# Kernel optimization log

Measured on AMD Instinct MI355X. Metric: run time of the kernel, lower is better.

The kernel has to match this reference:

```python
import jax, jax.numpy as jnp
import numpy as np


def _proj(W, b, x):
    # 1x1 conv == per-pixel GEMM over channels: [O,C] x [B,C,H,W] -> [B,O,H,W]
    return jnp.einsum('oc,bchw->bohw', W, x) + b[None, :, None, None]


def _cross(src, ctx, Wq, bq, Wk, bk, Wv, bv):
    # queries from src, keys/values from ctx; returns [B,C,H,W]
    B, C, H, W = src.shape
    HW = H * W
    q = _proj(Wq, bq, src).reshape(B, -1, HW)   # [B, C//8, HW]
    k = _proj(Wk, bk, ctx).reshape(B, -1, HW)   # [B, C//8, HW]
    v = _proj(Wv, bv, ctx).reshape(B, C, HW)    # [B, C,    HW]
    # attn[b,i,j] = softmax_j( q[b,:,i] . k[b,:,j] )
    attn = jax.nn.softmax(jnp.einsum('bci,bcj->bij', q, k), axis=-1)
    out = jnp.einsum('bcj,bij->bci', v, attn)   # [B, C, HW]
    return out.reshape(B, C, H, W)


def setup_inputs() -> dict:
    key = jax.random.key(0)
    ks = jax.random.split(key, 8)
    dim = 256
    B, H, W = 4, 64, 64
    return {
        'x': jax.random.normal(ks[0], (B, dim, H, W), jnp.float32),
        'y': jax.random.normal(ks[1], (B, dim, H, W), jnp.float32),
        'Wq': jax.random.normal(ks[2], (dim // 8, dim), jnp.float32) * 0.05,
        'bq': jax.random.normal(ks[3], (dim // 8,), jnp.float32) * 0.05,
        'Wk': jax.random.normal(ks[4], (dim // 8, dim), jnp.float32) * 0.05,
        'bk': jax.random.normal(ks[5], (dim // 8,), jnp.float32) * 0.05,
        'Wv': jax.random.normal(ks[6], (dim, dim), jnp.float32) * 0.05,
        'bv': jax.random.normal(ks[7], (dim,), jnp.float32) * 0.05,
    }


def reference(x, y, Wq, bq, Wk, bk, Wv, bv):
    outx = _cross(x, y, Wq, bq, Wk, bk, Wv, bv)  # x queries attend to y
    outy = _cross(y, x, Wq, bq, Wk, bk, Wv, bv)  # y queries attend to x
    return (outx, outy)
```

## Files before the change

### kernel.cpp

```cpp
#include <hip/hip_runtime.h>

#define BB 4
#define CC 256
#define DD 32
#define SS 4096

typedef __bf16 bf16;
typedef __bf16 bf16x8 __attribute__((ext_vector_type(8)));
typedef __bf16 bf16x4 __attribute__((ext_vector_type(4)));
typedef float f32x4 __attribute__((ext_vector_type(4)));
typedef unsigned int u32;
typedef u32 u32x4 __attribute__((ext_vector_type(4)));
typedef unsigned short u16;

#define Q_OFF  0
#define K_OFF  1048576
#define V_OFF  2097152
#define WB_OFF 10485760
#define CH_ELEM 16384

static __device__ __forceinline__ u32 pack2(float lo, float hi) {
    bf16 a = (bf16)lo, b = (bf16)hi;
    u16 ua = __builtin_bit_cast(u16, a), ub = __builtin_bit_cast(u16, b);
    return (u32)ua | ((u32)ub << 16);
}

static __device__ __forceinline__ void bar_vm12() {
    asm volatile("s_waitcnt vmcnt(12)" ::: "memory");
    __builtin_amdgcn_s_barrier();
    asm volatile("" ::: "memory");
}
static __device__ __forceinline__ void bar_plain() {
    asm volatile("" ::: "memory");
    __builtin_amdgcn_s_barrier();
    asm volatile("" ::: "memory");
}

__global__ __launch_bounds__(256) void prep_kernel(
    const float* __restrict__ x, const float* __restrict__ y,
    const float* __restrict__ Wq, const float* __restrict__ Wk,
    const float* __restrict__ Wv,
    bf16* __restrict__ xb, bf16* __restrict__ wb)
{
    const int t   = threadIdx.x;
    const int bid = blockIdx.x;

    if (bid >= 512) {
        const int gid = (bid - 512)*256 + t;
        const int idx = gid*8;
        const int o = idx >> 8, cc = idx & 255;
        const float* row = (o < 32) ? (Wq + (size_t)o*CC)
                         : (o < 64) ? (Wk + (size_t)(o-32)*CC)
                                    : (Wv + (size_t)(o-64)*CC);
        const float4 a = *(const float4*)(row + cc);
        const float4 c = *(const float4*)(row + cc + 4);
        bf16x8 pk;
        pk[0]=(bf16)a.x; pk[1]=(bf16)a.y; pk[2]=(bf16)a.z; pk[3]=(bf16)a.w;
        pk[4]=(bf16)c.x; pk[5]=(bf16)c.y; pk[6]=(bf16)c.z; pk[7]=(bf16)c.w;
        *(bf16x8*)(wb + idx) = pk;
        return;
    }

    const int dirb = bid & 7;
    const int src  = dirb >> 2;
    const int b    = dirb & 3;
    const int tile = bid >> 3;
    const float* in = (src ? y : x) + (size_t)b*CC*SS + tile*64;
    bf16* outp = xb + (size_t)dirb*1048576 + (size_t)tile*CH_ELEM;

    const int ln    = t & 15;
    const int quadf = (t >> 4) & 3;
    const int w     = t >> 6;
    #pragma unroll
    for (int cop = 0; cop < 2; ++cop) {
        const int co = w*2 + cop;
        #pragma unroll
        for (int pb = 0; pb < 4; ++pb) {
            float f[8];
            #pragma unroll
            for (int j = 0; j < 8; ++j)
                f[j] = in[(size_t)(8*quadf + 32*co + j)*SS + pb*16 + ln];
            bf16x8 pk;
            #pragma unroll
            for (int j = 0; j < 8; ++j) pk[j] = (bf16)f[j];
            *(bf16x8*)(outp + pb*4096 + co*512 + quadf*128 + ln*8) = pk;
        }
    }
}

__global__ __launch_bounds__(256, 2) void proj_all_kernel(
    const bf16* __restrict__ xb, const bf16* __restrict__ wb,
    const float* __restrict__ bq, const float* __restrict__ bk,
    const float* __restrict__ bv,
    bf16* __restrict__ qout, bf16* __restrict__ kout, bf16* __restrict__ vout)
{
    __shared__ __align__(16) char xsm[32768];

    const int t    = threadIdx.x;
    const int lane = t & 63;
    const int w    = t >> 6;
    const int ln   = lane & 15;
    const int quad = lane >> 4;

    const int bid  = blockIdx.x;
    const int dirb = bid & 7;
    const int src  = dirb >> 2;
    const int b    = dirb & 3;
    const int tile = bid >> 3;
    const int i0   = tile * 64;

    {
        const bf16* xstage = xb + (size_t)dirb*1048576 + (size_t)tile*CH_ELEM
                             + w*512 + lane*8;
        char* ldsb = xsm + w*1024;
        #pragma unroll
        for (int j = 0; j < 8; ++j)
            __builtin_amdgcn_global_load_lds(
                (const __attribute__((address_space(1))) void*)(xstage + j*2048),
                (__attribute__((address_space(3))) void*)(ldsb + j*4096),
                16, 0, 0);
    }

    float bias[5];
    #pragma unroll
    for (int nbl = 0; nbl < 5; ++nbl) {
        const int o = 80*w + nbl*16 + ln;
        bias[nbl] = (o < 32) ? bq[o] : (o < 64) ? bk[o-32] : bv[o-64];
    }
    const bf16* wrow = wb + (size_t)(80*w + ln)*CC + quad*8;
    bf16x8 bf[5];
    #pragma unroll
    for (int nbl = 0; nbl < 5; ++nbl)
        bf[nbl] = *(const bf16x8*)(wrow + (size_t)nbl*16*CC);

    f32x4 acc[4][5];
    #pragma unroll
    for (int mb = 0; mb < 4; ++mb)
        #pragma unroll
        for (int nbl = 0; nbl < 5; ++nbl)
            acc[mb][nbl] = (f32x4){bias[nbl], bias[nbl], bias[nbl], bias[nbl]};

    __syncthreads();

    for (int n = 0; n < 8; ++n) {
        bf16x8 af[4];
        #pragma unroll
        for (int mb = 0; mb < 4; ++mb)
            af[mb] = *(const bf16x8*)(xsm + mb*8192 + n*1024 + lane*16);
        #pragma unroll
        for (int mb = 0; mb < 4; ++mb)
            #pragma unroll
            for (int nbl = 0; nbl < 5; ++nbl)
                acc[mb][nbl] = __builtin_amdgcn_mfma_f32_16x16x32_bf16(
                                   af[mb], bf[nbl], acc[mb][nbl], 0, 0, 0);
        const int ccn = ((n+1)*32) & 255;
        #pragma unroll
        for (int nbl = 0; nbl < 5; ++nbl)
            bf[nbl] = *(const bf16x8*)(wrow + (size_t)nbl*16*CC + ccn);
    }

    bf16* qo = qout + (size_t)(src*BB + b)*SS*DD;
    bf16* ko = kout + (size_t)(src*BB + b)*SS*DD;
    bf16* vo = vout + (size_t)(src*BB + b)*CC*SS;
    const int n0 = tile;
    #pragma unroll
    for (int nbl = 0; nbl < 5; ++nbl) {
        const int o = 80*w + nbl*16 + ln;
        if (o < 32) {
            #pragma unroll
            for (int mb = 0; mb < 4; ++mb)
                #pragma unroll
                for (int r = 0; r < 4; ++r)
                    qo[(size_t)(i0 + mb*16 + quad*4 + r)*DD + o] = (bf16)acc[mb][nbl][r];
        } else if (o < 64) {
            #pragma unroll
            for (int mb = 0; mb < 4; ++mb)
                #pragma unroll
                for (int r = 0; r < 4; ++r)
                    ko[(size_t)(i0 + mb*16 + quad*4 + r)*DD + (o-32)] = (bf16)acc[mb][nbl][r];
        } else {
            const int c = o - 64;
            const int cb = c >> 4, cl = c & 15;
            #pragma unroll
            for (int mb = 0; mb < 4; ++mb) {
                bf16x4 pk;
                #pragma unroll
                for (int r = 0; r < 4; ++r) pk[r] = (bf16)acc[mb][nbl][r];
                *(bf16x4*)(vo + (size_t)(2*n0 + (mb>>1))*8192 + cb*512
                              + (quad*16 + cl)*8 + (mb&1)*4) = pk;
            }
        }
    }
}

#define L2E   1.4426950408889634f
#define SM_C  (16.0f * L2E)

__global__ __launch_bounds__(256, 2) void attn_kernel(
    const bf16* __restrict__ qg, const bf16* __restrict__ kg,
    const bf16* __restrict__ vg, float* __restrict__ out)
{
    __shared__ __align__(16) char vsm[2*32768];

    const int t    = threadIdx.x;
    const int lane = t & 63;
    const int w    = t >> 6;
    const int ln   = lane & 15;
    const int quad = lane >> 4;

    const int bid  = blockIdx.x;
    const int dirb = bid & 7;
    const int dir  = dirb >> 2;
    const int b    = dirb & 3;
    const int i0   = (bid >> 3) * 64;

    const bf16* q = qg + ((size_t)dir*BB + b)*SS*DD;
    const bf16* k = kg + ((size_t)(1-dir)*BB + b)*SS*DD;
    const bf16* v = vg + ((size_t)(1-dir)*BB + b)*(size_t)CC*SS;
    float* op = out + ((size_t)dir*BB + b)*(size_t)CC*SS;

    const bf16x8 bq = *(const bf16x8*)(q + (size_t)(i0 + w*16 + ln)*DD + quad*8);
    const bf16* kbase = k + (size_t)ln*DD + quad*8;
    const bf16* vstage = v + w*512 + lane*8;
    char* lds0 = vsm + w*1024;

    f32x4 o[16];
    #pragma unroll
    for (int cb = 0; cb < 16; ++cb) o[cb] = (f32x4){0.f,0.f,0.f,0.f};
    f32x4 lpq = (f32x4){0.f,0.f,0.f,0.f};

    bf16x8 kf[4];
    #pragma unroll
    for (int nb = 0; nb < 4; ++nb)
        kf[nb] = *(const bf16x8*)(kbase + (size_t)(nb*16)*DD);

    #define STAGE(ch, buf) do {                                               \
        const bf16* gp_ = vstage + (size_t)(ch)*CH_ELEM;                      \
        char* lp_ = lds0 + (buf)*32768;                                       \
        _Pragma("unroll")                                                     \
        for (int j = 0; j < 8; ++j)                                           \
            __builtin_amdgcn_global_load_lds(                                 \
                (const __attribute__((address_space(1))) void*)(gp_ + j*2048),\
                (__attribute__((address_space(3))) void*)(lp_ + j*4096),      \
                16, 0, 0);                                                    \
    } while (0)

    #define SMAX(sarr, pa) do {                                               \
        float e_[4][4];                                                       \
        _Pragma("unroll")                                                     \
        for (int nb = 0; nb < 4; ++nb)                                        \
            _Pragma("unroll")                                                 \
            for (int r = 0; r < 4; ++r) {                                     \
                e_[nb][r] = exp2f((sarr)[nb][r]*L2E - SM_C);                   \
                lpq[r] += e_[nb][r];                                          \
            }                                                                 \
        _Pragma("unroll")                                                     \
        for (int ks = 0; ks < 2; ++ks) {                                      \
            u32x4 pk_;                                                        \
            _Pragma("unroll")                                                 \
            for (int jp = 0; jp < 4; ++jp)                                    \
                pk_[jp] = pack2(e_[2*ks + (jp>>1)][2*(jp&1)],                 \
                                e_[2*ks + (jp>>1)][2*(jp&1) + 1]);            \
            (pa)[ks] = __builtin_bit_cast(bf16x8, pk_);                       \
        }                                                                     \
    } while (0)

    bf16x8 paA[2];
    {
        f32x4 s[4];
        #pragma unroll
        for (int nb = 0; nb < 4; ++nb)
            s[nb] = __builtin_amdgcn_mfma_f32_16x16x32_bf16(
                        kf[nb], bq, (f32x4){0.f,0.f,0.f,0.f}, 0, 0, 0);
        STAGE(0, 0);
        STAGE(1, 1);
        #pragma unroll
        for (int nb = 0; nb < 4; ++nb)
            kf[nb] = *(const bf16x8*)(kbase + (size_t)(64 + nb*16)*DD);
        SMAX(s, paA);
    }

    for (int n = 0; n < 64; ++n) {
        bar_vm12();

        const char* bufp = vsm + (n & 1)*32768;
        __builtin_amdgcn_s_setprio(1);
        #pragma unroll
        for (int st = 0; st < 32; ++st) {
            const int cb = st & 15;
            const bf16x8 vfr = *(const bf16x8*)(bufp + st*1024 + lane*16);
            o[cb] = __builtin_amdgcn_mfma_f32_16x16x32_bf16(
                        paA[st >> 4], vfr, o[cb], 0, 0, 0);
        }
        __builtin_amdgcn_s_setprio(0);

        f32x4 s[4];
        if (n < 63) {
            #pragma unroll
            for (int nb = 0; nb < 4; ++nb)
                s[nb] = __builtin_amdgcn_mfma_f32_16x16x32_bf16(
                            kf[nb], bq, (f32x4){0.f,0.f,0.f,0.f}, 0, 0, 0);
            const int j2 = ((n + 2) & 63) * 64;
            #pragma unroll
            for (int nb = 0; nb < 4; ++nb)
                kf[nb] = *(const bf16x8*)(kbase + (size_t)(j2 + nb*16)*DD);
        }

        bar_plain();
        if (n < 63)
            STAGE((n + 2) & 63, n & 1);

        if (n < 63)
            SMAX(s, paA);
    }

    float lp = (lpq[0] + lpq[1]) + (lpq[2] + lpq[3]);
    lp += __shfl_xor(lp, 16);
    lp += __shfl_xor(lp, 32);
    f32x4 ri;
    #pragma unroll
    for (int r = 0; r < 4; ++r)
        ri[r] = 1.0f / __shfl(lp, quad*4 + r);

    #pragma unroll
    for (int cb = 0; cb < 16; ++cb) {
        const int c = cb*16 + ln;
        float4 val = make_float4(o[cb][0]*ri[0], o[cb][1]*ri[1],
                                 o[cb][2]*ri[2], o[cb][3]*ri[3]);
        *(float4*)(op + (size_t)c*SS + i0 + w*16 + quad*4) = val;
    }
    #undef STAGE
    #undef SMAX
}

extern "C" void kernel_launch(void* const* d_in, const int* in_sizes, int n_in,
                              void* d_out, int out_size, void* d_ws, size_t ws_size,
                              hipStream_t stream)
{
    const float* x  = (const float*)d_in[0];
    const float* y  = (const float*)d_in[1];
    const float* Wq = (const float*)d_in[2];
    const float* bq = (const float*)d_in[3];
    const float* Wk = (const float*)d_in[4];
    const float* bk = (const float*)d_in[5];
    const float* Wv = (const float*)d_in[6];
    const float* bv = (const float*)d_in[7];
    float* out = (float*)d_out;
    bf16* ws   = (bf16*)d_ws;

    bf16* qw = ws + Q_OFF;
    bf16* kw = ws + K_OFF;
    bf16* vw = ws + V_OFF;
    bf16* wb = ws + WB_OFF;

    prep_kernel     <<<552, 256, 0, stream>>>(x, y, Wq, Wk, Wv, vw, wb);
    proj_all_kernel <<<512, 256, 0, stream>>>(vw, wb, bq, bk, bv, qw, kw, vw);
    attn_kernel     <<<512, 256, 0, stream>>>(qw, kw, vw, out);
}
```

Baseline: 223.7 us.

## Fuse input fp32-to-bf16 conversion into projection kernel via direct LDS staging

Removes the prep pass that converted x/y to bf16 in a tiled layout. The projection kernel now loads fp32 input tiles straight into LDS with global_load_lds and converts to bf16 while building MFMA fragments. Weight conversion moves to a small separate kernel. This cuts a full read/write round trip of the activations through global memory. In exchange it doubles LDS use to 64KB and adds strided scalar LDS reads plus conversions inside the MFMA loop, which may cause bank conflicts and lower occupancy.

```diff
diff --git a/kernel.cpp b/kernel.cpp
--- a/kernel.cpp
+++ b/kernel.cpp
@@ -36,65 +36,32 @@
     asm volatile("" ::: "memory");
 }
 
-__global__ __launch_bounds__(256) void prep_kernel(
+__global__ __launch_bounds__(256) void convert_w_kernel(
+    const float* __restrict__ Wq, const float* __restrict__ Wk,
+    const float* __restrict__ Wv, bf16* __restrict__ wb)
+{
+    const int gid = blockIdx.x*256 + threadIdx.x;
+    const int idx = gid*8;
+    const int o = idx >> 8, cc = idx & 255;
+    const float* row = (o < 32) ? (Wq + (size_t)o*CC)
+                     : (o < 64) ? (Wk + (size_t)(o-32)*CC)
+                                : (Wv + (size_t)(o-64)*CC);
+    const float4 a = *(const float4*)(row + cc);
+    const float4 c = *(const float4*)(row + cc + 4);
+    bf16x8 pk;
+    pk[0]=(bf16)a.x; pk[1]=(bf16)a.y; pk[2]=(bf16)a.z; pk[3]=(bf16)a.w;
+    pk[4]=(bf16)c.x; pk[5]=(bf16)c.y; pk[6]=(bf16)c.z; pk[7]=(bf16)c.w;
+    *(bf16x8*)(wb + idx) = pk;
+}
+
+__global__ __launch_bounds__(256, 2) void proj_all_kernel(
     const float* __restrict__ x, const float* __restrict__ y,
-    const float* __restrict__ Wq, const float* __restrict__ Wk,
-    const float* __restrict__ Wv,
-    bf16* __restrict__ xb, bf16* __restrict__ wb)
-{
-    const int t   = threadIdx.x;
-    const int bid = blockIdx.x;
-
-    if (bid >= 512) {
-        const int gid = (bid - 512)*256 + t;
-        const int idx = gid*8;
-        const int o = idx >> 8, cc = idx & 255;
-        const float* row = (o < 32) ? (Wq + (size_t)o*CC)
-                         : (o < 64) ? (Wk + (size_t)(o-32)*CC)
-                                    : (Wv + (size_t)(o-64)*CC);
-        const float4 a = *(const float4*)(row + cc);
-        const float4 c = *(const float4*)(row + cc + 4);
-        bf16x8 pk;
-        pk[0]=(bf16)a.x; pk[1]=(bf16)a.y; pk[2]=(bf16)a.z; pk[3]=(bf16)a.w;
-        pk[4]=(bf16)c.x; pk[5]=(bf16)c.y; pk[6]=(bf16)c.z; pk[7]=(bf16)c.w;
-        *(bf16x8*)(wb + idx) = pk;
-        return;
-    }
-
-    const int dirb = bid & 7;
-    const int src  = dirb >> 2;
-    const int b    = dirb & 3;
-    const int tile = bid >> 3;
-    const float* in = (src ? y : x) + (size_t)b*CC*SS + tile*64;
-    bf16* outp = xb + (size_t)dirb*1048576 + (size_t)tile*CH_ELEM;
-
-    const int ln    = t & 15;
-    const int quadf = (t >> 4) & 3;
-    const int w     = t >> 6;
-    #pragma unroll
-    for (int cop = 0; cop < 2; ++cop) {
-        const int co = w*2 + cop;
-        #pragma unroll
-        for (int pb = 0; pb < 4; ++pb) {
-            float f[8];
-            #pragma unroll
-            for (int j = 0; j < 8; ++j)
-                f[j] = in[(size_t)(8*quadf + 32*co + j)*SS + pb*16 + ln];
-            bf16x8 pk;
-            #pragma unroll
-            for (int j = 0; j < 8; ++j) pk[j] = (bf16)f[j];
-            *(bf16x8*)(outp + pb*4096 + co*512 + quadf*128 + ln*8) = pk;
-        }
-    }
-}
-
-__global__ __launch_bounds__(256, 2) void proj_all_kernel(
-    const bf16* __restrict__ xb, const bf16* __restrict__ wb,
+    const bf16* __restrict__ wb,
     const float* __restrict__ bq, const float* __restrict__ bk,
     const float* __restrict__ bv,
     bf16* __restrict__ qout, bf16* __restrict__ kout, bf16* __restrict__ vout)
 {
-    __shared__ __align__(16) char xsm[32768];
+    __shared__ __align__(16) char xsm[65536];
 
     const int t    = threadIdx.x;
     const int lane = t & 63;
@@ -109,15 +76,18 @@
     const int tile = bid >> 3;
     const int i0   = tile * 64;
 
+    const float* in = (src ? y : x) + (size_t)b*CC*SS + tile*64;
+
     {
-        const bf16* xstage = xb + (size_t)dirb*1048576 + (size_t)tile*CH_ELEM
-                             + w*512 + lane*8;
+        const int pos4 = (t & 15) * 4;
+        const int ccw  = t >> 4;
         char* ldsb = xsm + w*1024;
         #pragma unroll
-        for (int j = 0; j < 8; ++j)
+        for (int r = 0; r < 16; ++r)
             __builtin_amdgcn_global_load_lds(
-                (const __attribute__((address_space(1))) void*)(xstage + j*2048),
-                (__attribute__((address_space(3))) void*)(ldsb + j*4096),
+                (const __attribute__((address_space(1))) void*)
+                    (in + (size_t)(r*16 + ccw)*SS + pos4),
+                (__attribute__((address_space(3))) void*)(ldsb + r*4096),
                 16, 0, 0);
     }
 
@@ -142,11 +112,18 @@
 
     __syncthreads();
 
+    const float* xr = (const float*)xsm;
     for (int n = 0; n < 8; ++n) {
         bf16x8 af[4];
         #pragma unroll
-        for (int mb = 0; mb < 4; ++mb)
-            af[mb] = *(const bf16x8*)(xsm + mb*8192 + n*1024 + lane*16);
+        for (int mb = 0; mb < 4; ++mb) {
+            float f[8];
+            #pragma unroll
+            for (int j = 0; j < 8; ++j)
+                f[j] = xr[(n*32 + quad*8 + j)*64 + mb*16 + ln];
+            #pragma unroll
+            for (int j = 0; j < 8; ++j) af[mb][j] = (bf16)f[j];
+        }
         #pragma unroll
         for (int mb = 0; mb < 4; ++mb)
             #pragma unroll
@@ -353,7 +330,7 @@
     bf16* vw = ws + V_OFF;
     bf16* wb = ws + WB_OFF;
 
-    prep_kernel     <<<552, 256, 0, stream>>>(x, y, Wq, Wk, Wv, vw, wb);
-    proj_all_kernel <<<512, 256, 0, stream>>>(vw, wb, bq, bk, bv, qw, kw, vw);
+    convert_w_kernel<<<40,  256, 0, stream>>>(Wq, Wk, Wv, wb);
+    proj_all_kernel <<<512, 256, 0, stream>>>(x, y, wb, bq, bk, bv, qw, kw, vw);
     attn_kernel     <<<512, 256, 0, stream>>>(qw, kw, vw, out);
 }
```

Result: faster. 206.5 us (-7.7%).
